# Optimization experiments

Measured on AMD Instinct MI355X. Metric: run time of the kernel, lower is better.

The kernel has to match this reference:

```python
import jax, jax.numpy as jnp
import numpy as np

# Config mirrors module init: C=12 channels, include_time=True -> d=13, depth=3
# sig_channels = d + d^2 + d^3 = 2379

def setup_inputs() -> dict:
    key = jax.random.key(0)
    k1, k2, k3 = jax.random.split(key, 3)
    N, C, J, T, L = 8, 12, 25, 64, 5
    d = C + 1
    sig_channels = d + d * d + d ** 3  # 2379
    out_dim = 256
    x = jax.random.normal(k1, (N, C, J, T, L), dtype=jnp.float32)
    W = jax.random.normal(k2, (out_dim, sig_channels), dtype=jnp.float32) / np.sqrt(sig_channels)
    b = jax.random.normal(k3, (out_dim,), dtype=jnp.float32) * 0.01
    return {"x": x, "W": W, "b": b}


def _signature_depth3(path):
    """Truncated (depth 3) path signature with zero basepoint.
    path: [B, L, d] -> sig: [B, d + d^2 + d^3]
    Chen's identity: s <- s * exp(dx), with exp(dx)_n = dx^{(x)n} / n!
    """
    B, L, d = path.shape
    # basepoint=True: prepend zeros, then take increments
    inc = jnp.diff(jnp.concatenate([jnp.zeros((B, 1, d), path.dtype), path], axis=1), axis=1)  # [B, L, d]

    def step(carry, dx):
        s1, s2, s3 = carry  # [B,d], [B,d*d], [B,d^3]
        e2 = 0.5 * jnp.einsum('bi,bj->bij', dx, dx)                     # [B,d,d]
        e3 = (jnp.einsum('bij,bk->bijk', e2, dx) / 3.0).reshape(B, d ** 3)  # dx^3/6
        n1 = s1 + dx
        n2 = s2 + jnp.einsum('bi,bj->bij', s1, dx).reshape(B, d * d) + e2.reshape(B, d * d)
        n3 = (s3
              + jnp.einsum('bij,bk->bijk', s2.reshape(B, d, d), dx).reshape(B, d ** 3)
              + jnp.einsum('bi,bjk->bijk', s1, e2).reshape(B, d ** 3)
              + e3)
        return (n1, n2, n3), None

    init = (jnp.zeros((B, d), path.dtype),
            jnp.zeros((B, d * d), path.dtype),
            jnp.zeros((B, d ** 3), path.dtype))
    (s1, s2, s3), _ = jax.lax.scan(step, init, jnp.moveaxis(inc, 1, 0))
    return jnp.concatenate([s1, s2, s3], axis=-1)


def reference(x, W, b):
    N, C, J, T, L = x.shape
    B = J * T * N
    # windowed gather: block (i*T+j)*N..(..+1)*N = x[:,:,i,j,:].permute(0,2,1)
    path = jnp.transpose(x, (2, 3, 0, 4, 1)).reshape(B, L, C)  # [J*T*N, L, C]
    # Augment include_time=True: append time channel linspace(0,1,L)
    t = jnp.linspace(0.0, 1.0, L, dtype=path.dtype)
    path = jnp.concatenate([path, jnp.broadcast_to(t[None, :, None], (B, L, 1))], axis=-1)
    sig = _signature_depth3(path)                 # [B, 2379]
    z = sig @ W.T + b                             # [B, out_dim]
    # scatter back: res[:, :, i, j] = z[(i*T+j)*N : ...]
    return jnp.transpose(z.reshape(J, T, N, -1), (2, 3, 0, 1))  # [N, out_dim, J, T]
```

## Files before the change

kernel.cpp:

```cpp
#include <hip/hip_runtime.h>
#include <hip/hip_bf16.h>

typedef float f32x4 __attribute__((ext_vector_type(4)));
typedef short s16x8 __attribute__((ext_vector_type(8)));

#define SIGC 2379
#define KPAD 2432
#define NKT  76
#define SROW 2440
#define NPATH 12800


__device__ inline void split2(float v, __hip_bfloat16* h, __hip_bfloat16* l) {
    __hip_bfloat16 hh = __float2bfloat16(v);
    *h = hh;
    *l = __float2bfloat16(v - __bfloat162float(hh));
}

__device__ inline void gload_lds16(const __hip_bfloat16* g, __hip_bfloat16* l) {
    __builtin_amdgcn_global_load_lds(
        (const __attribute__((address_space(1))) void*)g,
        (__attribute__((address_space(3))) void*)l,
        16, 0, 0);
}

__global__ __launch_bounds__(256) void wconv_kernel(const float* __restrict__ W,
                                                    __hip_bfloat16* __restrict__ Wh,
                                                    __hip_bfloat16* __restrict__ Wl)
{
    int k = blockIdx.x * 256 + threadIdx.x;
    int n = blockIdx.y;
    if (k >= KPAD) return;
    float v = (k < SIGC) ? W[(size_t)n * SIGC + k] : 0.0f;
    size_t off = ((size_t)(n >> 4) * NKT + (k >> 5)) * 512 + ((k >> 3) & 3) * 128 + (n & 15) * 8 + (k & 7);
    split2(v, &Wh[off], &Wl[off]);
}

__global__ __launch_bounds__(256) void sig_kernel(const float* __restrict__ x,
                                                  __hip_bfloat16* __restrict__ Ah,
                                                  __hip_bfloat16* __restrict__ Al_,
                                                  int r_start)
{
    __shared__ float inc_s[4][5][16];
    __shared__ __align__(16) __hip_bfloat16 hi_s[4][SROW];
    __shared__ __align__(16) __hip_bfloat16 lo_s[4][SROW];

    const int t = threadIdx.x;
    const int w = t >> 6;
    const int lane = t & 63;

    const int p0 = lane;
    const int p1 = lane + 64;
    const int p2 = lane + 128;
    const bool has2 = (p2 < 169);
    const int i0 = p0 / 13, j0 = p0 - i0 * 13;
    const int i1 = p1 / 13, j1 = p1 - i1 * 13;
    const int i2 = p2 / 13, j2 = p2 - i2 * 13;

    for (int pp = 0; pp < 4; ++pp) {
        const int r = r_start + blockIdx.x * 16 + pp * 4 + w;
        const int nn = r & 7;
        const int jj = (r >> 3) & 63;
        const int ii = r >> 9;

        __syncthreads();
        if (lane < 13) {
            if (lane < 12) {
                const float* px = x + ((size_t)(nn * 12 + lane) * 1600 + ii * 64 + jj) * 5;
                float prev = 0.0f;
                #pragma unroll
                for (int l = 0; l < 5; ++l) {
                    float v = px[l];
                    inc_s[w][l][lane] = v - prev;
                    prev = v;
                }
            } else {
                inc_s[w][0][12] = 0.0f;
                #pragma unroll
                for (int l = 1; l < 5; ++l) inc_s[w][l][12] = 0.25f;
            }
        }
        __syncthreads();

        float s1i0 = 0.0f, s1i1 = 0.0f, s1i2 = 0.0f;
        float s2p0 = 0.0f, s2p1 = 0.0f, s2p2 = 0.0f;
        float s1own = 0.0f;
        float s3a[13], s3b[13], s3c[13];
        #pragma unroll
        for (int k = 0; k < 13; ++k) { s3a[k] = 0.0f; s3b[k] = 0.0f; s3c[k] = 0.0f; }

        for (int l = 0; l < 5; ++l) {
            float dxl[13];
            #pragma unroll
            for (int k = 0; k < 13; ++k) dxl[k] = inc_s[w][l][k];

            {
                float dxi = inc_s[w][l][i0];
                float dxj = inc_s[w][l][j0];
                float C   = s2p0 + 0.5f * dxj * (s1i0 + dxi * (1.0f / 3.0f));
                #pragma unroll
                for (int k = 0; k < 13; ++k) s3a[k] += dxl[k] * C;
                s2p0 += s1i0 * dxj + 0.5f * dxi * dxj;
                s1i0 += dxi;
            }
            {
                float dxi = inc_s[w][l][i1];
                float dxj = inc_s[w][l][j1];
                float C   = s2p1 + 0.5f * dxj * (s1i1 + dxi * (1.0f / 3.0f));
                #pragma unroll
                for (int k = 0; k < 13; ++k) s3b[k] += dxl[k] * C;
                s2p1 += s1i1 * dxj + 0.5f * dxi * dxj;
                s1i1 += dxi;
            }
            if (has2) {
                float dxi = inc_s[w][l][i2];
                float dxj = inc_s[w][l][j2];
                float C   = s2p2 + 0.5f * dxj * (s1i2 + dxi * (1.0f / 3.0f));
                #pragma unroll
                for (int k = 0; k < 13; ++k) s3c[k] += dxl[k] * C;
                s2p2 += s1i2 * dxj + 0.5f * dxi * dxj;
                s1i2 += dxi;
            }
            if (lane < 13) s1own += inc_s[w][l][lane];
        }

        if (lane < 13) split2(s1own, &hi_s[w][lane], &lo_s[w][lane]);
        split2(s2p0, &hi_s[w][13 + p0], &lo_s[w][13 + p0]);
        split2(s2p1, &hi_s[w][13 + p1], &lo_s[w][13 + p1]);
        if (has2) split2(s2p2, &hi_s[w][13 + p2], &lo_s[w][13 + p2]);
        #pragma unroll
        for (int k = 0; k < 13; ++k) split2(s3a[k], &hi_s[w][182 + p0 * 13 + k], &lo_s[w][182 + p0 * 13 + k]);
        #pragma unroll
        for (int k = 0; k < 13; ++k) split2(s3b[k], &hi_s[w][182 + p1 * 13 + k], &lo_s[w][182 + p1 * 13 + k]);
        if (has2) {
            #pragma unroll
            for (int k = 0; k < 13; ++k) split2(s3c[k], &hi_s[w][182 + p2 * 13 + k], &lo_s[w][182 + p2 * 13 + k]);
        }
        if (lane < KPAD - SIGC) {
            hi_s[w][SIGC + lane] = __float2bfloat16(0.0f);
            lo_s[w][SIGC + lane] = __float2bfloat16(0.0f);
        }

        __syncthreads();

        const int rtl = blockIdx.x;
        const int rr = t & 3, ks = (t >> 2) & 3, ts = t >> 4;
        #pragma unroll
        for (int it2 = 0; it2 < 5; ++it2) {
            int kt = it2 * 16 + ts;
            if (kt < NKT) {
                size_t off = ((size_t)rtl * NKT + kt) * 512 + ks * 128 + (pp * 4 + rr) * 8;
                int lidx = kt * 32 + ks * 8;
                *reinterpret_cast<int4*>(Ah + off)  = *reinterpret_cast<const int4*>(&hi_s[rr][lidx]);
                *reinterpret_cast<int4*>(Al_ + off) = *reinterpret_cast<const int4*>(&lo_s[rr][lidx]);
            }
        }
    }
}

__global__ __launch_bounds__(256) void gemm_kernel(const __hip_bfloat16* __restrict__ Ah,
                                                   const __hip_bfloat16* __restrict__ Al_,
                                                   const __hip_bfloat16* __restrict__ Wh,
                                                   const __hip_bfloat16* __restrict__ Wl,
                                                   const float* __restrict__ b,
                                                   float* __restrict__ out,
                                                   int r_start, int nmblk)
{
    __shared__ __align__(16) __hip_bfloat16 L[3][32 * 512];

    const int bid = blockIdx.x;
    const int x8 = bid & 7;
    const int h = (bid >> 3) & 1;
    const int q = bid >> 4;
    const int mIdx = q * 8 + x8;
    if (mIdx >= nmblk) return;

    const int t = threadIdx.x;
    const int lane = t & 63;
    const int w = t >> 6;
    const int wm = w >> 1, wn = w & 1;
    const int rt0 = mIdx * 8;
    const int nt0 = h * 8;

    f32x4 acc[4][4] = {};

    auto stage = [&](int buf, int kt) {
        #pragma unroll
        for (int s = 0; s < 8; ++s) {
            int tt = w * 8 + s;
            const __hip_bfloat16* g;
            if (tt < 8)       g = Ah  + ((size_t)(rt0 + tt)       * NKT + kt) * 512;
            else if (tt < 16) g = Al_ + ((size_t)(rt0 + tt - 8)   * NKT + kt) * 512;
            else if (tt < 24) g = Wh  + ((size_t)(nt0 + tt - 16)  * NKT + kt) * 512;
            else              g = Wl  + ((size_t)(nt0 + tt - 24)  * NKT + kt) * 512;
            gload_lds16(g + lane * 8, &L[buf][tt * 512]);
        }
    };

    auto compute = [&](int lb) {
        const __hip_bfloat16* Lb = &L[lb][0];
        s16x8 ah[4], al4[4], bh[4], bl4[4];
        #pragma unroll
        for (int mm = 0; mm < 4; ++mm) {
            ah[mm]  = *reinterpret_cast<const s16x8*>(&Lb[(wm * 4 + mm) * 512 + lane * 8]);
            al4[mm] = *reinterpret_cast<const s16x8*>(&Lb[(8 + wm * 4 + mm) * 512 + lane * 8]);
        }
        #pragma unroll
        for (int nn = 0; nn < 4; ++nn) {
            bh[nn]  = *reinterpret_cast<const s16x8*>(&Lb[(16 + wn * 4 + nn) * 512 + lane * 8]);
            bl4[nn] = *reinterpret_cast<const s16x8*>(&Lb[(24 + wn * 4 + nn) * 512 + lane * 8]);
        }
        __builtin_amdgcn_s_setprio(1);
        #pragma unroll
        for (int nn = 0; nn < 4; ++nn)
            #pragma unroll
            for (int mm = 0; mm < 4; ++mm) {
                acc[mm][nn] = __builtin_amdgcn_mfma_f32_16x16x32_bf16(ah[mm],  bh[nn],  acc[mm][nn], 0, 0, 0);
                acc[mm][nn] = __builtin_amdgcn_mfma_f32_16x16x32_bf16(ah[mm],  bl4[nn], acc[mm][nn], 0, 0, 0);
                acc[mm][nn] = __builtin_amdgcn_mfma_f32_16x16x32_bf16(al4[mm], bh[nn],  acc[mm][nn], 0, 0, 0);
            }
        __builtin_amdgcn_s_setprio(0);
    };

    stage(0, 0);
    stage(1, 1);
    int b0 = 0, b1 = 1, b2 = 2;

    #pragma unroll 1
    for (int kt = 0; kt < NKT; ++kt) {
        if (kt + 2 < NKT) {
            stage(b2, kt + 2);
            asm volatile("s_waitcnt vmcnt(16)" ::: "memory");
        } else if (kt + 1 < NKT) {
            asm volatile("s_waitcnt vmcnt(8)" ::: "memory");
        } else {
            asm volatile("s_waitcnt vmcnt(0)" ::: "memory");
        }
        __builtin_amdgcn_s_barrier();
        compute(b0);
        __builtin_amdgcn_s_barrier();
        int tmp = b0; b0 = b1; b1 = b2; b2 = tmp;
    }

    __syncthreads();
    float* T = (float*)&L[0][0];
    #pragma unroll
    for (int mm = 0; mm < 4; ++mm)
        #pragma unroll
        for (int nn = 0; nn < 4; ++nn)
            #pragma unroll
            for (int rr = 0; rr < 4; ++rr) {
                int p = wm * 64 + mm * 16 + (lane >> 4) * 4 + rr;
                int o = wn * 64 + nn * 16 + (lane & 15);
                T[p * 132 + o] = acc[mm][nn][rr];
            }
    __syncthreads();

    const int pbase = r_start + mIdx * 128;
    const int ii = pbase >> 9;
    const int jj0 = (pbase >> 3) & 63;
    const int ol = t >> 1, hh = t & 1;
    const int o = h * 128 + ol;
    const float bo = b[o];
    #pragma unroll
    for (int c = 0; c < 4; ++c) {
        int ni = hh * 4 + c;
        float v[16];
        #pragma unroll
        for (int qq = 0; qq < 16; ++qq) v[qq] = T[(qq * 8 + ni) * 132 + ol] + bo;
        float* dst = out + (size_t)(ni * 256 + o) * 1600 + ii * 64 + jj0;
        *reinterpret_cast<float4*>(dst)      = make_float4(v[0],  v[1],  v[2],  v[3]);
        *reinterpret_cast<float4*>(dst + 4)  = make_float4(v[4],  v[5],  v[6],  v[7]);
        *reinterpret_cast<float4*>(dst + 8)  = make_float4(v[8],  v[9],  v[10], v[11]);
        *reinterpret_cast<float4*>(dst + 12) = make_float4(v[12], v[13], v[14], v[15]);
    }
}

extern "C" void kernel_launch(void* const* d_in, const int* in_sizes, int n_in,
                              void* d_out, int out_size, void* d_ws, size_t ws_size,
                              hipStream_t stream)
{
    const float* x = (const float*)d_in[0];
    const float* W = (const float*)d_in[1];
    const float* b = (const float*)d_in[2];
    float* out = (float*)d_out;

    char* ws = (char*)d_ws;
    __hip_bfloat16* Wh = (__hip_bfloat16*)ws;
    __hip_bfloat16* Wl = Wh + (size_t)16 * NKT * 512;
    size_t a_off = (((size_t)16 * NKT * 512 * 2 * 2) + 255) & ~(size_t)255;

    size_t avail = (ws_size > a_off) ? ws_size - a_off : 0;
    long long maxp = (long long)(avail / ((size_t)KPAD * 4));
    int chunk = (int)((maxp / 128) * 128);
    if (chunk > NPATH) chunk = NPATH;
    if (chunk < 128) chunk = 128;

    __hip_bfloat16* Ah = (__hip_bfloat16*)(ws + a_off);
    __hip_bfloat16* Al_ = Ah + (size_t)chunk * KPAD;

    wconv_kernel<<<dim3(10, 256), 256, 0, stream>>>(W, Wh, Wl);

    for (int r0 = 0; r0 < NPATH; r0 += chunk) {
        int cnt = NPATH - r0;
        if (cnt > chunk) cnt = chunk;
        int nmblk = cnt / 128;
        int nblk = ((nmblk + 7) / 8) * 16;
        sig_kernel<<<dim3(cnt / 16), 256, 0, stream>>>(x, Ah, Al_, r0);
        gemm_kernel<<<dim3(nblk), 256, 0, stream>>>(Ah, Al_, Wh, Wl, b, out, r0, nmblk);
    }
}
```

Before: 113.0 us.

## Shrink GEMM blocks to single wavefront with 64x128 tiles, drop barriers

The GEMM kernel now uses one 64-thread wavefront per block, computing a 64x128 output tile instead of a 128x128 tile split over four waves. Because a single wave owns the whole LDS buffer, all block barriers and syncthreads are removed, and the vmcnt waits are rescaled for 24 loads per stage. This doubles the number of blocks, which improves CU occupancy and load balance for 12800 paths. The cost is more global traffic for W tiles per output, since W is reused across fewer rows, and each wave must issue all the loads itself.

```diff
diff --git a/kernel.cpp b/kernel.cpp
--- a/kernel.cpp
+++ b/kernel.cpp
@@ -158,15 +158,15 @@
     }
 }
 
-__global__ __launch_bounds__(256) void gemm_kernel(const __hip_bfloat16* __restrict__ Ah,
-                                                   const __hip_bfloat16* __restrict__ Al_,
-                                                   const __hip_bfloat16* __restrict__ Wh,
-                                                   const __hip_bfloat16* __restrict__ Wl,
-                                                   const float* __restrict__ b,
-                                                   float* __restrict__ out,
-                                                   int r_start, int nmblk)
+__global__ __launch_bounds__(64) void gemm_kernel(const __hip_bfloat16* __restrict__ Ah,
+                                                  const __hip_bfloat16* __restrict__ Al_,
+                                                  const __hip_bfloat16* __restrict__ Wh,
+                                                  const __hip_bfloat16* __restrict__ Wl,
+                                                  const float* __restrict__ b,
+                                                  float* __restrict__ out,
+                                                  int r_start, int nmblk)
 {
-    __shared__ __align__(16) __hip_bfloat16 L[3][32 * 512];
+    __shared__ __align__(16) __hip_bfloat16 L[3][24 * 512];
 
     const int bid = blockIdx.x;
     const int x8 = bid & 7;
@@ -175,51 +175,53 @@
     const int mIdx = q * 8 + x8;
     if (mIdx >= nmblk) return;
 
-    const int t = threadIdx.x;
-    const int lane = t & 63;
-    const int w = t >> 6;
-    const int wm = w >> 1, wn = w & 1;
-    const int rt0 = mIdx * 8;
+    const int lane = threadIdx.x;
+    const int rt0 = mIdx * 4;
     const int nt0 = h * 8;
 
-    f32x4 acc[4][4] = {};
+    f32x4 acc[4][8] = {};
 
     auto stage = [&](int buf, int kt) {
-        #pragma unroll
-        for (int s = 0; s < 8; ++s) {
-            int tt = w * 8 + s;
-            const __hip_bfloat16* g;
-            if (tt < 8)       g = Ah  + ((size_t)(rt0 + tt)       * NKT + kt) * 512;
-            else if (tt < 16) g = Al_ + ((size_t)(rt0 + tt - 8)   * NKT + kt) * 512;
-            else if (tt < 24) g = Wh  + ((size_t)(nt0 + tt - 16)  * NKT + kt) * 512;
-            else              g = Wl  + ((size_t)(nt0 + tt - 24)  * NKT + kt) * 512;
-            gload_lds16(g + lane * 8, &L[buf][tt * 512]);
-        }
+        __hip_bfloat16* Lb = &L[buf][0];
+        #pragma unroll
+        for (int s = 0; s < 4; ++s)
+            gload_lds16(Ah  + ((size_t)(rt0 + s) * NKT + kt) * 512 + lane * 8, Lb + s * 512);
+        #pragma unroll
+        for (int s = 0; s < 4; ++s)
+            gload_lds16(Al_ + ((size_t)(rt0 + s) * NKT + kt) * 512 + lane * 8, Lb + (4 + s) * 512);
+        #pragma unroll
+        for (int s = 0; s < 8; ++s)
+            gload_lds16(Wh  + ((size_t)(nt0 + s) * NKT + kt) * 512 + lane * 8, Lb + (8 + s) * 512);
+        #pragma unroll
+        for (int s = 0; s < 8; ++s)
+            gload_lds16(Wl  + ((size_t)(nt0 + s) * NKT + kt) * 512 + lane * 8, Lb + (16 + s) * 512);
     };
 
-    auto compute = [&](int lb) {
-        const __hip_bfloat16* Lb = &L[lb][0];
-        s16x8 ah[4], al4[4], bh[4], bl4[4];
+    auto compute = [&](int buf) {
+        const __hip_bfloat16* Lb = &L[buf][0];
+        s16x8 ah[4], al4[4];
         #pragma unroll
         for (int mm = 0; mm < 4; ++mm) {
-            ah[mm]  = *reinterpret_cast<const s16x8*>(&Lb[(wm * 4 + mm) * 512 + lane * 8]);
-            al4[mm] = *reinterpret_cast<const s16x8*>(&Lb[(8 + wm * 4 + mm) * 512 + lane * 8]);
-        }
-        #pragma unroll
-        for (int nn = 0; nn < 4; ++nn) {
-            bh[nn]  = *reinterpret_cast<const s16x8*>(&Lb[(16 + wn * 4 + nn) * 512 + lane * 8]);
-            bl4[nn] = *reinterpret_cast<const s16x8*>(&Lb[(24 + wn * 4 + nn) * 512 + lane * 8]);
-        }
-        __builtin_amdgcn_s_setprio(1);
-        #pragma unroll
-        for (int nn = 0; nn < 4; ++nn)
-            #pragma unroll
-            for (int mm = 0; mm < 4; ++mm) {
-                acc[mm][nn] = __builtin_amdgcn_mfma_f32_16x16x32_bf16(ah[mm],  bh[nn],  acc[mm][nn], 0, 0, 0);
-                acc[mm][nn] = __builtin_amdgcn_mfma_f32_16x16x32_bf16(ah[mm],  bl4[nn], acc[mm][nn], 0, 0, 0);
-                acc[mm][nn] = __builtin_amdgcn_mfma_f32_16x16x32_bf16(al4[mm], bh[nn],  acc[mm][nn], 0, 0, 0);
-            }
-        __builtin_amdgcn_s_setprio(0);
+            ah[mm]  = *reinterpret_cast<const s16x8*>(&Lb[mm * 512 + lane * 8]);
+            al4[mm] = *reinterpret_cast<const s16x8*>(&Lb[(4 + mm) * 512 + lane * 8]);
+        }
+        #pragma unroll
+        for (int nh = 0; nh < 2; ++nh) {
+            s16x8 bh[4], bl4[4];
+            #pragma unroll
+            for (int nn = 0; nn < 4; ++nn) {
+                bh[nn]  = *reinterpret_cast<const s16x8*>(&Lb[(8 + nh * 4 + nn) * 512 + lane * 8]);
+                bl4[nn] = *reinterpret_cast<const s16x8*>(&Lb[(16 + nh * 4 + nn) * 512 + lane * 8]);
+            }
+            #pragma unroll
+            for (int nn = 0; nn < 4; ++nn)
+                #pragma unroll
+                for (int mm = 0; mm < 4; ++mm) {
+                    acc[mm][nh * 4 + nn] = __builtin_amdgcn_mfma_f32_16x16x32_bf16(ah[mm],  bh[nn],  acc[mm][nh * 4 + nn], 0, 0, 0);
+                    acc[mm][nh * 4 + nn] = __builtin_amdgcn_mfma_f32_16x16x32_bf16(ah[mm],  bl4[nn], acc[mm][nh * 4 + nn], 0, 0, 0);
+                    acc[mm][nh * 4 + nn] = __builtin_amdgcn_mfma_f32_16x16x32_bf16(al4[mm], bh[nn],  acc[mm][nh * 4 + nn], 0, 0, 0);
+                }
+        }
     };
 
     stage(0, 0);
@@ -230,49 +232,45 @@
     for (int kt = 0; kt < NKT; ++kt) {
         if (kt + 2 < NKT) {
             stage(b2, kt + 2);
-            asm volatile("s_waitcnt vmcnt(16)" ::: "memory");
+            asm volatile("s_waitcnt vmcnt(48)" ::: "memory");
         } else if (kt + 1 < NKT) {
-            asm volatile("s_waitcnt vmcnt(8)" ::: "memory");
+            asm volatile("s_waitcnt vmcnt(24)" ::: "memory");
         } else {
             asm volatile("s_waitcnt vmcnt(0)" ::: "memory");
         }
-        __builtin_amdgcn_s_barrier();
         compute(b0);
-        __builtin_amdgcn_s_barrier();
         int tmp = b0; b0 = b1; b1 = b2; b2 = tmp;
     }
 
-    __syncthreads();
     float* T = (float*)&L[0][0];
     #pragma unroll
     for (int mm = 0; mm < 4; ++mm)
         #pragma unroll
-        for (int nn = 0; nn < 4; ++nn)
+        for (int nn = 0; nn < 8; ++nn)
             #pragma unroll
             for (int rr = 0; rr < 4; ++rr) {
-                int p = wm * 64 + mm * 16 + (lane >> 4) * 4 + rr;
-                int o = wn * 64 + nn * 16 + (lane & 15);
+                int p = mm * 16 + (lane >> 4) * 4 + rr;
+                int o = nn * 16 + (lane & 15);
                 T[p * 132 + o] = acc[mm][nn][rr];
             }
-    __syncthreads();
-
-    const int pbase = r_start + mIdx * 128;
+
+    const int pbase = r_start + mIdx * 64;
     const int ii = pbase >> 9;
     const int jj0 = (pbase >> 3) & 63;
-    const int ol = t >> 1, hh = t & 1;
-    const int o = h * 128 + ol;
-    const float bo = b[o];
     #pragma unroll
-    for (int c = 0; c < 4; ++c) {
-        int ni = hh * 4 + c;
-        float v[16];
-        #pragma unroll
-        for (int qq = 0; qq < 16; ++qq) v[qq] = T[(qq * 8 + ni) * 132 + ol] + bo;
-        float* dst = out + (size_t)(ni * 256 + o) * 1600 + ii * 64 + jj0;
-        *reinterpret_cast<float4*>(dst)      = make_float4(v[0],  v[1],  v[2],  v[3]);
-        *reinterpret_cast<float4*>(dst + 4)  = make_float4(v[4],  v[5],  v[6],  v[7]);
-        *reinterpret_cast<float4*>(dst + 8)  = make_float4(v[8],  v[9],  v[10], v[11]);
-        *reinterpret_cast<float4*>(dst + 12) = make_float4(v[12], v[13], v[14], v[15]);
+    for (int o2 = 0; o2 < 2; ++o2) {
+        int col = o2 * 64 + lane;
+        int o = h * 128 + col;
+        float bo = b[o];
+        #pragma unroll
+        for (int ni = 0; ni < 8; ++ni) {
+            float v[8];
+            #pragma unroll
+            for (int qq = 0; qq < 8; ++qq) v[qq] = T[(qq * 8 + ni) * 132 + col] + bo;
+            float* dst = out + (size_t)(ni * 256 + o) * 1600 + ii * 64 + jj0;
+            *reinterpret_cast<float4*>(dst)     = make_float4(v[0], v[1], v[2], v[3]);
+            *reinterpret_cast<float4*>(dst + 4) = make_float4(v[4], v[5], v[6], v[7]);
+        }
     }
 }
 
@@ -304,9 +302,9 @@
     for (int r0 = 0; r0 < NPATH; r0 += chunk) {
         int cnt = NPATH - r0;
         if (cnt > chunk) cnt = chunk;
-        int nmblk = cnt / 128;
+        int nmblk = cnt / 64;
         int nblk = ((nmblk + 7) / 8) * 16;
         sig_kernel<<<dim3(cnt / 16), 256, 0, stream>>>(x, Ah, Al_, r0);
-        gemm_kernel<<<dim3(nblk), 256, 0, stream>>>(Ah, Al_, Wh, Wl, b, out, r0, nmblk);
+        gemm_kernel<<<dim3(nblk), 64, 0, stream>>>(Ah, Al_, Wh, Wl, b, out, r0, nmblk);
     }
 }
```

Result: slower. 142.2 us (+25.8%).
